# Kernel tuning notes

Hardware: AMD Instinct MI355X
Metric: run time of the kernel (lower is better)

## Reference

```python
import jax, jax.numpy as jnp
import numpy as np

HIDDEN = 1024
N_HEADS = 16
HEAD_DIM = HIDDEN // N_HEADS  # 64
SCALE = HEAD_DIM ** -0.5
B, QL, KVL = 2, 2048, 4096


def setup_inputs() -> dict:
    key = jax.random.key(0)
    ks = jax.random.split(key, 7)
    s = 0.02
    return {
        "query_states": jax.random.normal(ks[0], (B, QL, HIDDEN), jnp.float32),
        "key_states": jax.random.normal(ks[1], (B, KVL, HIDDEN), jnp.float32),
        "value_states": jax.random.normal(ks[2], (B, KVL, HIDDEN), jnp.float32),
        # torch nn.Linear weights: shape [out, in], applied as x @ W.T
        "Wq": jax.random.normal(ks[3], (HIDDEN, HIDDEN), jnp.float32) * s,
        "Wk": jax.random.normal(ks[4], (HIDDEN, HIDDEN), jnp.float32) * s,
        "Wv": jax.random.normal(ks[5], (HIDDEN, HIDDEN), jnp.float32) * s,
        "Wo": jax.random.normal(ks[6], (HIDDEN, HIDDEN), jnp.float32) * s,
    }


def reference(query_states, key_states, value_states, Wq, Wk, Wv, Wo):
    b, ql, _ = query_states.shape
    kvl = key_states.shape[1]
    # projections (torch Linear: x @ W.T)
    q = query_states @ Wq.T  # [b, ql, H]
    k = key_states @ Wk.T    # [b, kvl, H]
    v = value_states @ Wv.T  # [b, kvl, H]
    # split heads -> [b, h, s, d]
    q = q.reshape(b, ql, N_HEADS, HEAD_DIM).transpose(0, 2, 1, 3)
    k = k.reshape(b, kvl, N_HEADS, HEAD_DIM).transpose(0, 2, 1, 3)
    v = v.reshape(b, kvl, N_HEADS, HEAD_DIM).transpose(0, 2, 1, 3)
    # scores [b, h, ql, kvl]
    scores = jnp.einsum("bhqd,bhkd->bhqk", q, k) * SCALE
    attn = jax.nn.softmax(scores, axis=-1)
    out = jnp.einsum("bhqk,bhkd->bhqd", attn, v)  # [b, h, ql, d]
    out = out.transpose(0, 2, 1, 3).reshape(b, ql, HIDDEN)
    return out @ Wo.T
```

## Files before the change

### kernel.cpp

```cpp
#include <hip/hip_runtime.h>

#define HID   1024
#define NH    16
#define HD    64
#define QL    2048
#define KVL   4096
#define NB    2
#define QSCALE 0.180336880111120426f

typedef short s8v  __attribute__((ext_vector_type(8)));
typedef short s4v  __attribute__((ext_vector_type(4)));
typedef float f4v  __attribute__((ext_vector_type(4)));

__device__ __forceinline__ unsigned short f2bf(float f) {
  unsigned int u = __builtin_bit_cast(unsigned int, f);
  u += 0x7FFFu + ((u >> 16) & 1u);
  return (unsigned short)(u >> 16);
}

__device__ __forceinline__ float fexp2(float x) {
#if __has_builtin(__builtin_amdgcn_exp2f)
  return __builtin_amdgcn_exp2f(x);
#else
  return exp2f(x);
#endif
}

__global__ __launch_bounds__(256)
void cast_all(const float* __restrict__ q, const float* __restrict__ k,
              const float* __restrict__ v, const float* __restrict__ wq,
              const float* __restrict__ wk, const float* __restrict__ wv,
              const float* __restrict__ wo, unsigned short* __restrict__ dst) {
  size_t c = (size_t)blockIdx.x * 256 + threadIdx.x;
  const float* src; size_t lc; float sc = 1.0f;
  if (c < 524288)       { src = q;  lc = c; }
  else if (c < 1572864) { src = k;  lc = c - 524288; }
  else if (c < 2621440) { src = v;  lc = c - 1572864; }
  else if (c < 2752512) { src = wq; lc = c - 2621440; sc = QSCALE; }
  else if (c < 2883584) { src = wk; lc = c - 2752512; }
  else if (c < 3014656) { src = wv; lc = c - 2883584; }
  else                  { src = wo; lc = c - 3014656; }
  const float4* p = (const float4*)(src + lc * 8);
  float4 a = p[0], b = p[1];
  union { s8v v8; unsigned short h[8]; } u;
  u.h[0] = f2bf(a.x * sc); u.h[1] = f2bf(a.y * sc);
  u.h[2] = f2bf(a.z * sc); u.h[3] = f2bf(a.w * sc);
  u.h[4] = f2bf(b.x * sc); u.h[5] = f2bf(b.y * sc);
  u.h[6] = f2bf(b.z * sc); u.h[7] = f2bf(b.w * sc);
  *(s8v*)(dst + c * 8) = u.v8;
}

typedef const __attribute__((address_space(1))) unsigned int* gas_t;
typedef __attribute__((address_space(3))) unsigned int*       las_t;

__device__ __forceinline__ void gl_lds16(const unsigned short* g, unsigned short* l) {
  __builtin_amdgcn_global_load_lds((gas_t)(const void*)g, (las_t)(void*)l, 16, 0, 0);
}

template <bool OUT_BF16>
__device__ __forceinline__ void gemm_body(const unsigned short* __restrict__ A,
                                          const unsigned short* __restrict__ B,
                                          void* __restrict__ Cv, int N, int K,
                                          int bx, int by,
                                          unsigned short (*As)[128 * 32],
                                          unsigned short (*Bs)[128 * 32]) {
  const int tid  = threadIdx.x;
  const int wave = tid >> 6, lane = tid & 63;
  const int wm = wave >> 1, wn = wave & 1;
  const int quad = lane >> 4, l15 = lane & 15;
  const int row0 = by * 128;
  const int col0 = bx * 128;
  const int srow = lane >> 2;
  const int scol = (lane & 3) * 8;

  f4v acc[4][4] = {};

#define G_STAGE(KI, BI)                                                         \
  {                                                                             \
    _Pragma("unroll")                                                           \
    for (int cc = 0; cc < 2; cc++) {                                            \
      int c = wave + cc * 4;                                                    \
      gl_lds16(A + (size_t)(row0 + c * 16 + srow) * K + (KI) * 32 + scol,       \
               &As[BI][c * 512]);                                               \
      gl_lds16(B + (size_t)(col0 + c * 16 + srow) * K + (KI) * 32 + scol,       \
               &Bs[BI][c * 512]);                                               \
    }                                                                           \
  }

  const int nk = K >> 5;
  G_STAGE(0, 0);
  __syncthreads();

  for (int ki = 0; ki < nk; ki++) {
    const int cur = ki & 1;
    if (ki + 1 < nk) G_STAGE(ki + 1, 1 - cur);

    s8v af[4], bf[4];
#pragma unroll
    for (int i = 0; i < 4; i++)
      af[i] = *(const s8v*)&As[cur][(wm * 64 + i * 16 + l15) * 32 + quad * 8];
#pragma unroll
    for (int j = 0; j < 4; j++)
      bf[j] = *(const s8v*)&Bs[cur][(wn * 64 + j * 16 + l15) * 32 + quad * 8];
#pragma unroll
    for (int i = 0; i < 4; i++)
#pragma unroll
      for (int j = 0; j < 4; j++)
        acc[i][j] = __builtin_amdgcn_mfma_f32_16x16x32_bf16(af[i], bf[j],
                                                            acc[i][j], 0, 0, 0);
    __syncthreads();
  }
#undef G_STAGE

#pragma unroll
  for (int i = 0; i < 4; i++) {
#pragma unroll
    for (int j = 0; j < 4; j++) {
      int r = row0 + wm * 64 + i * 16 + quad * 4;
      int c = col0 + wn * 64 + j * 16 + l15;
#pragma unroll
      for (int reg = 0; reg < 4; reg++) {
        float v = acc[i][j][reg];
        if constexpr (OUT_BF16)
          ((unsigned short*)Cv)[(size_t)(r + reg) * N + c] = f2bf(v);
        else
          ((float*)Cv)[(size_t)(r + reg) * N + c] = v;
      }
    }
  }
}

__global__ __launch_bounds__(256, 2)
void proj_fused(const unsigned short* __restrict__ qc, const unsigned short* __restrict__ kc,
                const unsigned short* __restrict__ vc, const unsigned short* __restrict__ wqc,
                const unsigned short* __restrict__ wkc, const unsigned short* __restrict__ wvc,
                unsigned short* __restrict__ qp, unsigned short* __restrict__ kp,
                unsigned short* __restrict__ vpt) {
  __shared__ unsigned short As[2][128 * 32];
  __shared__ unsigned short Bs[2][128 * 32];
  int bid = blockIdx.x;
  if (bid < 256) {
    gemm_body<true>(qc, wqc, qp, HID, HID, bid & 7, bid >> 3, As, Bs);
  } else if (bid < 768) {
    int l = bid - 256;
    gemm_body<true>(kc, wkc, kp, HID, HID, l & 7, l >> 3, As, Bs);
  } else {
    int l = bid - 768;
    int b = l >> 8, r = l & 255;
    gemm_body<true>(wvc, vc + (size_t)b * KVL * HID,
                    vpt + (size_t)b * HID * KVL, KVL, HID, r & 31, r >> 5, As, Bs);
  }
}

__global__ __launch_bounds__(256, 2)
void o_gemm(const unsigned short* __restrict__ ao, const unsigned short* __restrict__ woc,
            float* __restrict__ out) {
  __shared__ unsigned short As[2][128 * 32];
  __shared__ unsigned short Bs[2][128 * 32];
  int bid = blockIdx.x;
  gemm_body<false>(ao, woc, out, HID, HID, bid & 7, bid >> 3, As, Bs);
}

#define LDSK 40

template <typename T>
__device__ __forceinline__ void stage_tile(unsigned short* dst, const T* src,
                                           int ld, int tid, float sc) {
#pragma unroll
  for (int rep = 0; rep < 2; rep++) {
    int s = rep * 256 + tid;
    int row = s >> 2;
    int cs  = (s & 3) * 8;
    const T* p = src + (size_t)row * ld + cs;
    s8v val;
    if constexpr (sizeof(T) == 4) {
      float4 f0 = *(const float4*)p;
      float4 f1 = *(const float4*)(p + 4);
      union { s8v v; unsigned short h[8]; } u;
      u.h[0] = f2bf(f0.x * sc); u.h[1] = f2bf(f0.y * sc);
      u.h[2] = f2bf(f0.z * sc); u.h[3] = f2bf(f0.w * sc);
      u.h[4] = f2bf(f1.x * sc); u.h[5] = f2bf(f1.y * sc);
      u.h[6] = f2bf(f1.z * sc); u.h[7] = f2bf(f1.w * sc);
      val = u.v;
    } else {
      val = *(const s8v*)p;
    }
    *(s8v*)&dst[row * LDSK + cs] = val;
  }
}

template <typename TA, typename TB, bool OUT_BF16>
__global__ __launch_bounds__(256)
void gemm_conv(const TA* __restrict__ A, const TB* __restrict__ B,
               void* __restrict__ Cv, int M, int N, int K, float bscale,
               long long bz, long long cz) {
  __shared__ unsigned short As[128 * LDSK];
  __shared__ unsigned short Bs[128 * LDSK];
  const TB* Bp = B + (size_t)blockIdx.z * (size_t)bz;
  const int tid  = threadIdx.x;
  const int wave = tid >> 6, lane = tid & 63;
  const int wm = wave >> 1, wn = wave & 1;
  const int quad = lane >> 4, l15 = lane & 15;
  const int row0 = blockIdx.y * 128;
  const int col0 = blockIdx.x * 128;

  f4v acc[4][4] = {};

  for (int k0 = 0; k0 < K; k0 += 32) {
    __syncthreads();
    stage_tile(As, A + (size_t)row0 * K + k0, K, tid, 1.0f);
    stage_tile(Bs, Bp + (size_t)col0 * K + k0, K, tid, bscale);
    __syncthreads();

    s8v af[4], bf[4];
#pragma unroll
    for (int i = 0; i < 4; i++)
      af[i] = *(const s8v*)&As[(wm * 64 + i * 16 + l15) * LDSK + quad * 8];
#pragma unroll
    for (int j = 0; j < 4; j++)
      bf[j] = *(const s8v*)&Bs[(wn * 64 + j * 16 + l15) * LDSK + quad * 8];
#pragma unroll
    for (int i = 0; i < 4; i++)
#pragma unroll
      for (int j = 0; j < 4; j++)
        acc[i][j] = __builtin_amdgcn_mfma_f32_16x16x32_bf16(af[i], bf[j],
                                                            acc[i][j], 0, 0, 0);
  }

  char* Cp = (char*)Cv + (size_t)blockIdx.z * (size_t)cz * (OUT_BF16 ? 2 : 4);
#pragma unroll
  for (int i = 0; i < 4; i++) {
#pragma unroll
    for (int j = 0; j < 4; j++) {
      int r = row0 + wm * 64 + i * 16 + quad * 4;
      int c = col0 + wn * 64 + j * 16 + l15;
#pragma unroll
      for (int reg = 0; reg < 4; reg++) {
        float v = acc[i][j][reg];
        if constexpr (OUT_BF16)
          ((unsigned short*)Cp)[(size_t)(r + reg) * N + c] = f2bf(v);
        else
          ((float*)Cp)[(size_t)(r + reg) * N + c] = v;
      }
    }
  }
}

#define AST 72

__global__ __launch_bounds__(256, 2)
void attn5(const unsigned short* __restrict__ qp,
           const unsigned short* __restrict__ kp,
           const unsigned short* __restrict__ vpt,
           unsigned short* __restrict__ ao) {
  __shared__ unsigned short Ks[2][64 * 64];
  __shared__ unsigned short Vt[2][64 * 64];
  __shared__ unsigned short Pt[4][32 * AST];

  const int bid  = blockIdx.x;
  const int qb   = bid & 15;
  const int h    = (bid >> 4) & 15;
  const int b    = bid >> 8;
  const int tid  = threadIdx.x;
  const int wave = tid >> 6, lane = tid & 63;
  const int quad = lane >> 4, l15 = lane & 15;
  const int q0   = qb * 128 + wave * 32;

  const unsigned short* kbase = kp + (size_t)b * KVL * HID + h * HD;
  const unsigned short* vbase = vpt + (size_t)(b * NH + h) * HD * KVL;

  int prow[2], pcol[2], pbase[2];
#pragma unroll
  for (int i = 0; i < 2; i++) {
    int p = (i * 4 + wave) * 64 + lane;
    prow[i]  = p >> 3;
    pcol[i]  = ((p & 7) ^ (prow[i] & 7)) * 8;
    pbase[i] = (i * 4 + wave) * 512;
  }

  s8v qf[2][2];
#pragma unroll
  for (int qt = 0; qt < 2; qt++) {
    const size_t qrow = (size_t)(b * QL + q0 + qt * 16 + l15) * HID + h * HD;
#pragma unroll
    for (int ks = 0; ks < 2; ks++)
      qf[qt][ks] = *(const s8v*)(qp + qrow + ks * 32 + quad * 8);
  }

  float lrun[2] = {0.f, 0.f};
  f4v oacc[2][4] = {};

#define STAGE_KV(KT, BI)                                                        \
  {                                                                             \
    const unsigned short* kb = kbase + (size_t)((KT) * 64) * HID;               \
    const unsigned short* vb = vbase + (KT) * 64;                               \
    _Pragma("unroll")                                                           \
    for (int i = 0; i < 2; i++) {                                               \
      gl_lds16(kb + (size_t)prow[i] * HID + pcol[i], &Ks[BI][pbase[i]]);        \
      gl_lds16(vb + (size_t)prow[i] * KVL + pcol[i], &Vt[BI][pbase[i]]);        \
    }                                                                           \
  }

  constexpr int NT = KVL / 64;
  STAGE_KV(0, 0);
  __syncthreads();

  for (int kt = 0; kt < NT; kt++) {
    const int cur = kt & 1;
    if (kt + 1 < NT) STAGE_KV(kt + 1, 1 - cur);

    f4v sacc[2][4] = {};
#pragma unroll
    for (int ks = 0; ks < 2; ks++)
#pragma unroll
      for (int mt = 0; mt < 4; mt++) {
        int row = mt * 16 + l15;
        int xc  = ((ks * 4 + quad) ^ (row & 7)) * 8;
        s8v kf = *(const s8v*)&Ks[cur][row * 64 + xc];
#pragma unroll
        for (int qt = 0; qt < 2; qt++)
          sacc[qt][mt] = __builtin_amdgcn_mfma_f32_16x16x32_bf16(kf, qf[qt][ks],
                                                                 sacc[qt][mt], 0, 0, 0);
      }

#pragma unroll
    for (int qt = 0; qt < 2; qt++) {
      float rs = 0.f;
#pragma unroll
      for (int mt = 0; mt < 4; mt++) {
        float p0 = fexp2(sacc[qt][mt][0]);
        float p1 = fexp2(sacc[qt][mt][1]);
        float p2 = fexp2(sacc[qt][mt][2]);
        float p3 = fexp2(sacc[qt][mt][3]);
        rs += (p0 + p1) + (p2 + p3);
        union { s4v v4; unsigned short hh[4]; } pk;
        pk.hh[0] = f2bf(p0); pk.hh[1] = f2bf(p1);
        pk.hh[2] = f2bf(p2); pk.hh[3] = f2bf(p3);
        *(s4v*)&Pt[wave][(qt * 16 + l15) * AST + mt * 16 + quad * 4] = pk.v4;
      }
      rs += __shfl_xor(rs, 16, 64);
      rs += __shfl_xor(rs, 32, 64);
      lrun[qt] += rs;
    }

#pragma unroll
    for (int ch = 0; ch < 2; ch++) {
      s8v vf[4];
#pragma unroll
      for (int dt = 0; dt < 4; dt++) {
        int row = dt * 16 + l15;
        int xc  = ((ch * 4 + quad) ^ (row & 7)) * 8;
        vf[dt] = *(const s8v*)&Vt[cur][row * 64 + xc];
      }
#pragma unroll
      for (int qt = 0; qt < 2; qt++) {
        s8v pf = *(const s8v*)&Pt[wave][(qt * 16 + l15) * AST + ch * 32 + quad * 8];
#pragma unroll
        for (int dt = 0; dt < 4; dt++)
          oacc[qt][dt] = __builtin_amdgcn_mfma_f32_16x16x32_bf16(pf, vf[dt],
                                                                 oacc[qt][dt], 0, 0, 0);
      }
    }

    __syncthreads();
  }
#undef STAGE_KV

#pragma unroll
  for (int qt = 0; qt < 2; qt++) {
    float li = 1.0f / lrun[qt];
    float lr[4];
#pragma unroll
    for (int r = 0; r < 4; r++)
      lr[r] = __shfl(li, (lane & 48) + quad * 4 + r, 64);
#pragma unroll
    for (int dt = 0; dt < 4; dt++)
#pragma unroll
      for (int r = 0; r < 4; r++) {
        int qq = q0 + qt * 16 + quad * 4 + r;
        int cc = h * HD + dt * 16 + l15;
        ao[(size_t)(b * QL + qq) * HID + cc] = f2bf(oacc[qt][dt][r] * lr[r]);
      }
  }
}

extern "C" void kernel_launch(void* const* d_in, const int* in_sizes, int n_in,
                              void* d_out, int out_size, void* d_ws, size_t ws_size,
                              hipStream_t stream) {
  const float* q  = (const float*)d_in[0];
  const float* k  = (const float*)d_in[1];
  const float* v  = (const float*)d_in[2];
  const float* Wq = (const float*)d_in[3];
  const float* Wk = (const float*)d_in[4];
  const float* Wv = (const float*)d_in[5];
  const float* Wo = (const float*)d_in[6];
  float* out = (float*)d_out;
  char* ws = (char*)d_ws;
  dim3 blk(256);

  const long long MB = 1024 * 1024;
  if (ws_size >= (size_t)88 * MB) {
    unsigned short* qc  = (unsigned short*)(ws);
    unsigned short* kc  = (unsigned short*)(ws + 8 * MB);
    unsigned short* vc  = (unsigned short*)(ws + 24 * MB);
    unsigned short* wqc = (unsigned short*)(ws + 40 * MB);
    unsigned short* wkc = (unsigned short*)(ws + 42 * MB);
    unsigned short* wvc = (unsigned short*)(ws + 44 * MB);
    unsigned short* woc = (unsigned short*)(ws + 46 * MB);
    unsigned short* qp  = (unsigned short*)(ws + 48 * MB);
    unsigned short* kp  = (unsigned short*)(ws + 56 * MB);
    unsigned short* vpt = (unsigned short*)(ws + 72 * MB);
    unsigned short* ao  = (unsigned short*)(ws);

    cast_all<<<12288, blk, 0, stream>>>(q, k, v, Wq, Wk, Wv, Wo, (unsigned short*)ws);
    proj_fused<<<1280, blk, 0, stream>>>(qc, kc, vc, wqc, wkc, wvc, qp, kp, vpt);
    attn5<<<512, blk, 0, stream>>>(qp, kp, vpt, ao);
    o_gemm<<<256, blk, 0, stream>>>(ao, woc, out);
  } else {
    unsigned short* qp  = (unsigned short*)(ws);
    unsigned short* kp  = (unsigned short*)(ws + 8 * MB);
    unsigned short* vpt = (unsigned short*)(ws + 24 * MB);
    unsigned short* ao  = (unsigned short*)(ws + 40 * MB);

    gemm_conv<float, float, true><<<dim3(8, 32), blk, 0, stream>>>(q, Wq, qp, NB * QL, HID, HID, QSCALE, 0, 0);
    gemm_conv<float, float, true><<<dim3(8, 64), blk, 0, stream>>>(k, Wk, kp, NB * KVL, HID, HID, 1.0f, 0, 0);
    gemm_conv<float, float, true><<<dim3(32, 8, 2), blk, 0, stream>>>(Wv, v, vpt, HID, KVL, HID, 1.0f,
                                                                      (long long)KVL * HID, (long long)HID * KVL);
    attn5<<<512, blk, 0, stream>>>(qp, kp, vpt, ao);
    gemm_conv<unsigned short, float, false><<<dim3(8, 32), blk, 0, stream>>>(ao, Wo, out, NB * QL, HID, HID, 1.0f, 0, 0);
  }
}
```

Before: 335.1 us.

## Widen attention query tile, split KV in halves with combine kernel

The attention kernel now gives each wave 64 query rows instead of 32, doubling reuse of each staged K/V tile. To keep 512 blocks in flight it splits the KV sequence into two halves and writes unnormalized bf16 partial outputs plus row sums, which a new combine kernel adds and normalizes. It also swaps round-to-nearest for truncation when packing P to bf16, moves the P buffer to an XOR-swizzled layout, and raises the occupancy hint on the GEMM kernels. The cost is extra register pressure, a second bf16 rounding of partials, more global traffic and one more launch. There is no max subtraction, so the split relies on the softmax being unshifted.

Result: faster. 309.0 us (-7.8%).

```diff
diff --git a/kernel.cpp b/kernel.cpp
--- a/kernel.cpp
+++ b/kernel.cpp
@@ -17,7 +17,10 @@
   u += 0x7FFFu + ((u >> 16) & 1u);
   return (unsigned short)(u >> 16);
 }
-
+__device__ __forceinline__ float bf2f(unsigned short h) {
+  unsigned int u = ((unsigned int)h) << 16;
+  return __builtin_bit_cast(float, u);
+}
 __device__ __forceinline__ float fexp2(float x) {
 #if __has_builtin(__builtin_amdgcn_exp2f)
   return __builtin_amdgcn_exp2f(x);
@@ -130,7 +133,7 @@
   }
 }
 
-__global__ __launch_bounds__(256, 2)
+__global__ __launch_bounds__(256, 4)
 void proj_fused(const unsigned short* __restrict__ qc, const unsigned short* __restrict__ kc,
                 const unsigned short* __restrict__ vc, const unsigned short* __restrict__ wqc,
                 const unsigned short* __restrict__ wkc, const unsigned short* __restrict__ wvc,
@@ -152,7 +155,7 @@
   }
 }
 
-__global__ __launch_bounds__(256, 2)
+__global__ __launch_bounds__(256, 4)
 void o_gemm(const unsigned short* __restrict__ ao, const unsigned short* __restrict__ woc,
             float* __restrict__ out) {
   __shared__ unsigned short As[2][128 * 32];
@@ -246,28 +249,32 @@
   }
 }
 
-#define AST 72
-
+template <bool SPLIT>
 __global__ __launch_bounds__(256, 2)
-void attn5(const unsigned short* __restrict__ qp,
+void attn6(const unsigned short* __restrict__ qp,
            const unsigned short* __restrict__ kp,
            const unsigned short* __restrict__ vpt,
+           unsigned short* __restrict__ po,
+           float* __restrict__ pl,
            unsigned short* __restrict__ ao) {
   __shared__ unsigned short Ks[2][64 * 64];
   __shared__ unsigned short Vt[2][64 * 64];
-  __shared__ unsigned short Pt[4][32 * AST];
+  __shared__ unsigned short Pt[4][64 * 64];
 
   const int bid  = blockIdx.x;
-  const int qb   = bid & 15;
-  const int h    = (bid >> 4) & 15;
-  const int b    = bid >> 8;
+  const int qb   = bid & 7;
+  const int h    = (bid >> 3) & 15;
+  const int b    = (bid >> 7) & 1;
+  const int half = SPLIT ? (bid >> 8) : 0;
   const int tid  = threadIdx.x;
   const int wave = tid >> 6, lane = tid & 63;
   const int quad = lane >> 4, l15 = lane & 15;
-  const int q0   = qb * 128 + wave * 32;
-
-  const unsigned short* kbase = kp + (size_t)b * KVL * HID + h * HD;
-  const unsigned short* vbase = vpt + (size_t)(b * NH + h) * HD * KVL;
+  const int q0   = qb * 256 + wave * 64;
+  const int kvoff = half * (KVL / 2);
+  const int NT   = SPLIT ? (KVL / 128) : (KVL / 64);
+
+  const unsigned short* kbase = kp + (size_t)b * KVL * HID + h * HD + (size_t)kvoff * HID;
+  const unsigned short* vbase = vpt + (size_t)(b * NH + h) * HD * KVL + kvoff;
 
   int prow[2], pcol[2], pbase[2];
 #pragma unroll
@@ -278,17 +285,17 @@
     pbase[i] = (i * 4 + wave) * 512;
   }
 
-  s8v qf[2][2];
-#pragma unroll
-  for (int qt = 0; qt < 2; qt++) {
-    const size_t qrow = (size_t)(b * QL + q0 + qt * 16 + l15) * HID + h * HD;
+  s8v qf[4][2];
+#pragma unroll
+  for (int nt = 0; nt < 4; nt++) {
+    const size_t qrow = (size_t)(b * QL + q0 + nt * 16 + l15) * HID + h * HD;
 #pragma unroll
     for (int ks = 0; ks < 2; ks++)
-      qf[qt][ks] = *(const s8v*)(qp + qrow + ks * 32 + quad * 8);
-  }
-
-  float lrun[2] = {0.f, 0.f};
-  f4v oacc[2][4] = {};
+      qf[nt][ks] = *(const s8v*)(qp + qrow + ks * 32 + quad * 8);
+  }
+
+  float lrun[4] = {0.f, 0.f, 0.f, 0.f};
+  f4v oacc[4][4] = {};
 
 #define STAGE_KV(KT, BI)                                                        \
   {                                                                             \
@@ -301,7 +308,6 @@
     }                                                                           \
   }
 
-  constexpr int NT = KVL / 64;
   STAGE_KV(0, 0);
   __syncthreads();
 
@@ -309,7 +315,7 @@
     const int cur = kt & 1;
     if (kt + 1 < NT) STAGE_KV(kt + 1, 1 - cur);
 
-    f4v sacc[2][4] = {};
+    f4v sacc[4][4] = {};
 #pragma unroll
     for (int ks = 0; ks < 2; ks++)
 #pragma unroll
@@ -318,29 +324,34 @@
         int xc  = ((ks * 4 + quad) ^ (row & 7)) * 8;
         s8v kf = *(const s8v*)&Ks[cur][row * 64 + xc];
 #pragma unroll
-        for (int qt = 0; qt < 2; qt++)
-          sacc[qt][mt] = __builtin_amdgcn_mfma_f32_16x16x32_bf16(kf, qf[qt][ks],
-                                                                 sacc[qt][mt], 0, 0, 0);
-      }
-
-#pragma unroll
-    for (int qt = 0; qt < 2; qt++) {
+        for (int nt = 0; nt < 4; nt++)
+          sacc[mt][nt] = __builtin_amdgcn_mfma_f32_16x16x32_bf16(kf, qf[nt][ks],
+                                                                 sacc[mt][nt], 0, 0, 0);
+      }
+
+#pragma unroll
+    for (int nt = 0; nt < 4; nt++) {
       float rs = 0.f;
 #pragma unroll
       for (int mt = 0; mt < 4; mt++) {
-        float p0 = fexp2(sacc[qt][mt][0]);
-        float p1 = fexp2(sacc[qt][mt][1]);
-        float p2 = fexp2(sacc[qt][mt][2]);
-        float p3 = fexp2(sacc[qt][mt][3]);
+        float p0 = fexp2(sacc[mt][nt][0]);
+        float p1 = fexp2(sacc[mt][nt][1]);
+        float p2 = fexp2(sacc[mt][nt][2]);
+        float p3 = fexp2(sacc[mt][nt][3]);
         rs += (p0 + p1) + (p2 + p3);
         union { s4v v4; unsigned short hh[4]; } pk;
-        pk.hh[0] = f2bf(p0); pk.hh[1] = f2bf(p1);
-        pk.hh[2] = f2bf(p2); pk.hh[3] = f2bf(p3);
-        *(s4v*)&Pt[wave][(qt * 16 + l15) * AST + mt * 16 + quad * 4] = pk.v4;
+        pk.hh[0] = (unsigned short)(__builtin_bit_cast(unsigned int, p0) >> 16);
+        pk.hh[1] = (unsigned short)(__builtin_bit_cast(unsigned int, p1) >> 16);
+        pk.hh[2] = (unsigned short)(__builtin_bit_cast(unsigned int, p2) >> 16);
+        pk.hh[3] = (unsigned short)(__builtin_bit_cast(unsigned int, p3) >> 16);
+        int row = nt * 16 + l15;
+        int c   = mt * 2 + (quad >> 1);
+        int off = ((c ^ (row & 7)) * 8) + (quad & 1) * 4;
+        *(s4v*)&Pt[wave][row * 64 + off] = pk.v4;
       }
       rs += __shfl_xor(rs, 16, 64);
       rs += __shfl_xor(rs, 32, 64);
-      lrun[qt] += rs;
+      lrun[nt] += rs;
     }
 
 #pragma unroll
@@ -353,8 +364,10 @@
         vf[dt] = *(const s8v*)&Vt[cur][row * 64 + xc];
       }
 #pragma unroll
-      for (int qt = 0; qt < 2; qt++) {
-        s8v pf = *(const s8v*)&Pt[wave][(qt * 16 + l15) * AST + ch * 32 + quad * 8];
+      for (int qt = 0; qt < 4; qt++) {
+        int row = qt * 16 + l15;
+        int xc  = ((ch * 4 + quad) ^ (row & 7)) * 8;
+        s8v pf = *(const s8v*)&Pt[wave][row * 64 + xc];
 #pragma unroll
         for (int dt = 0; dt < 4; dt++)
           oacc[qt][dt] = __builtin_amdgcn_mfma_f32_16x16x32_bf16(pf, vf[dt],
@@ -366,22 +379,60 @@
   }
 #undef STAGE_KV
 
-#pragma unroll
-  for (int qt = 0; qt < 2; qt++) {
-    float li = 1.0f / lrun[qt];
-    float lr[4];
-#pragma unroll
-    for (int r = 0; r < 4; r++)
-      lr[r] = __shfl(li, (lane & 48) + quad * 4 + r, 64);
-#pragma unroll
-    for (int dt = 0; dt < 4; dt++)
-#pragma unroll
-      for (int r = 0; r < 4; r++) {
-        int qq = q0 + qt * 16 + quad * 4 + r;
-        int cc = h * HD + dt * 16 + l15;
-        ao[(size_t)(b * QL + qq) * HID + cc] = f2bf(oacc[qt][dt][r] * lr[r]);
-      }
-  }
+  if constexpr (SPLIT) {
+    unsigned short* pob = po + (size_t)half * NB * QL * HID;
+#pragma unroll
+    for (int qt = 0; qt < 4; qt++) {
+#pragma unroll
+      for (int dt = 0; dt < 4; dt++)
+#pragma unroll
+        for (int r = 0; r < 4; r++) {
+          int qq = q0 + qt * 16 + quad * 4 + r;
+          int cc = h * HD + dt * 16 + l15;
+          pob[(size_t)(b * QL + qq) * HID + cc] = f2bf(oacc[qt][dt][r]);
+        }
+      if (quad == 0)
+        pl[(size_t)half * NB * NH * QL + (b * NH + h) * QL + q0 + qt * 16 + l15] = lrun[qt];
+    }
+  } else {
+#pragma unroll
+    for (int qt = 0; qt < 4; qt++) {
+      float li = 1.0f / lrun[qt];
+      float lr[4];
+#pragma unroll
+      for (int r = 0; r < 4; r++)
+        lr[r] = __shfl(li, (lane & 48) + quad * 4 + r, 64);
+#pragma unroll
+      for (int dt = 0; dt < 4; dt++)
+#pragma unroll
+        for (int r = 0; r < 4; r++) {
+          int qq = q0 + qt * 16 + quad * 4 + r;
+          int cc = h * HD + dt * 16 + l15;
+          ao[(size_t)(b * QL + qq) * HID + cc] = f2bf(oacc[qt][dt][r] * lr[r]);
+        }
+    }
+  }
+}
+
+__global__ __launch_bounds__(256)
+void combine(const unsigned short* __restrict__ po, const float* __restrict__ pl,
+             unsigned short* __restrict__ ao) {
+  int t  = blockIdx.x * 256 + threadIdx.x;
+  int r  = t >> 7;
+  int c8 = t & 127;
+  int b = r >> 11, q = r & 2047, h = c8 >> 3;
+  size_t lidx = (size_t)(b * NH + h) * QL + q;
+  float l = pl[lidx] + pl[(size_t)NB * NH * QL + lidx];
+  float inv = 1.0f / l;
+  size_t off = (size_t)r * HID + c8 * 8;
+  s8v a = *(const s8v*)(po + off);
+  s8v c = *(const s8v*)(po + (size_t)NB * QL * HID + off);
+  union { s8v v8; unsigned short hh[8]; } ua, uc, uo;
+  ua.v8 = a; uc.v8 = c;
+#pragma unroll
+  for (int e = 0; e < 8; e++)
+    uo.hh[e] = f2bf((bf2f(ua.hh[e]) + bf2f(uc.hh[e])) * inv);
+  *(s8v*)(ao + off) = uo.v8;
 }
 
 extern "C" void kernel_launch(void* const* d_in, const int* in_sizes, int n_in,
@@ -411,10 +462,13 @@
     unsigned short* kp  = (unsigned short*)(ws + 56 * MB);
     unsigned short* vpt = (unsigned short*)(ws + 72 * MB);
     unsigned short* ao  = (unsigned short*)(ws);
+    unsigned short* po  = (unsigned short*)(ws + 8 * MB);
+    float*          pl  = (float*)(ws + 40 * MB);
 
     cast_all<<<12288, blk, 0, stream>>>(q, k, v, Wq, Wk, Wv, Wo, (unsigned short*)ws);
     proj_fused<<<1280, blk, 0, stream>>>(qc, kc, vc, wqc, wkc, wvc, qp, kp, vpt);
-    attn5<<<512, blk, 0, stream>>>(qp, kp, vpt, ao);
+    attn6<true><<<512, blk, 0, stream>>>(qp, kp, vpt, po, pl, nullptr);
+    combine<<<2048, blk, 0, stream>>>(po, pl, ao);
     o_gemm<<<256, blk, 0, stream>>>(ao, woc, out);
   } else {
     unsigned short* qp  = (unsigned short*)(ws);
@@ -426,7 +480,7 @@
     gemm_conv<float, float, true><<<dim3(8, 64), blk, 0, stream>>>(k, Wk, kp, NB * KVL, HID, HID, 1.0f, 0, 0);
     gemm_conv<float, float, true><<<dim3(32, 8, 2), blk, 0, stream>>>(Wv, v, vpt, HID, KVL, HID, 1.0f,
                                                                       (long long)KVL * HID, (long long)HID * KVL);
-    attn5<<<512, blk, 0, stream>>>(qp, kp, vpt, ao);
+    attn6<false><<<256, blk, 0, stream>>>(qp, kp, vpt, nullptr, nullptr, ao);
     gemm_conv<unsigned short, float, false><<<dim3(8, 32), blk, 0, stream>>>(ao, Wo, out, NB * QL, HID, HID, 1.0f, 0, 0);
   }
 }
```
